# Kernel tuning notes

Hardware: AMD Instinct MI355X
Metric: run time of the kernel (lower is better)

## Reference

```python
import jax, jax.numpy as jnp
import numpy as np

B, C, H, Wd = 4096, 32, 14, 14
ENC_DIM = 512
ATT_DIM = 128


def setup_inputs() -> dict:
    key = jax.random.key(0)
    ks = jax.random.split(key, 10)
    s = 0.05
    return {
        "img_features": jax.random.normal(ks[0], (B, C, H, Wd), jnp.float32),
        "prev_hidden": jax.random.normal(ks[1], (B, ENC_DIM), jnp.float32),
        "W_w": jax.random.normal(ks[2], (ATT_DIM, C), jnp.float32) * s,
        "W_b": jnp.zeros((ATT_DIM,), jnp.float32),
        "U_w": jax.random.normal(ks[3], (ATT_DIM, ENC_DIM), jnp.float32) * s,
        "U_b": jnp.zeros((ATT_DIM,), jnp.float32),
        "v_w": jax.random.normal(ks[4], (1, ATT_DIM), jnp.float32) * s,
        "v_b": jnp.zeros((1,), jnp.float32),
        "fb_w": jax.random.normal(ks[5], (C, ENC_DIM), jnp.float32) * s,
        "fb_b": jnp.zeros((C,), jnp.float32),
    }


def reference(img_features, prev_hidden, W_w, W_b, U_w, U_b, v_w, v_b, fb_w, fb_b):
    b = img_features.shape[0]
    c = img_features.shape[1]
    # [B, C, H, W] -> [B, P, C] where P = H*W (spatial positions)
    img_parts = img_features.reshape(b, c, -1).transpose(0, 2, 1)
    W_s = jnp.einsum('bpc,ac->bpa', img_parts, W_w) + W_b          # [B, P, 128]
    U_h = prev_hidden @ U_w.T + U_b                                 # [B, 128]
    att = jnp.tanh(W_s + U_h[:, None, :])                           # [B, P, 128]
    score = jnp.einsum('bpa,a->bp', att, v_w[0]) + v_b[0]           # [B, P]
    att_weights = jax.nn.softmax(score, axis=1)                     # softmax over spatial
    context = jnp.einsum('bpc,bp->bc', img_parts, att_weights)      # [B, 32]
    beta = jax.nn.sigmoid(prev_hidden @ fb_w.T + fb_b)              # [B, 32]
    context = context * beta
    return (context, att_weights)
```

## Files before the change

kernel.cpp:

```cpp
#include <hip/hip_runtime.h>
#include <hip/hip_bf16.h>


typedef __attribute__((ext_vector_type(8))) short short8;
typedef __attribute__((ext_vector_type(8))) __bf16 bf16x8;
typedef __attribute__((ext_vector_type(4))) float floatx4;
typedef __attribute__((ext_vector_type(4))) unsigned int uint4v;

#define K2E 2.8853900817779268f

#if __has_builtin(__builtin_amdgcn_exp2f)
#define EXP2F(x) __builtin_amdgcn_exp2f(x)
#else
#define EXP2F(x) __expf(0.6931471805599453f * (x))
#endif

static __device__ __forceinline__ float bf2f(unsigned short u) {
    union { unsigned int i; float f; } v; v.i = ((unsigned int)u) << 16; return v.f;
}
static __device__ __forceinline__ unsigned short f2bf(float f) {
    union { float f; unsigned int i; } v; v.f = f;
    unsigned int r = v.i + 0x7FFFu + ((v.i >> 16) & 1u);
    return (unsigned short)(r >> 16);
}
static __device__ __forceinline__ float sigmoid_rcp(float x) {
    return __builtin_amdgcn_rcpf(1.0f + __expf(-x));
}
static __device__ __forceinline__ void split_trunc8(const float* src, bf16x8* hi, bf16x8* lo) {
    uint4v u0 = *(const uint4v*)src;
    uint4v u1 = *(const uint4v*)(src + 4);
    unsigned int fb[8], lb[8];
#pragma unroll
    for (int j = 0; j < 4; j++) { fb[j] = u0[j]; fb[4 + j] = u1[j]; }
#pragma unroll
    for (int k = 0; k < 8; k++) {
        float x = __uint_as_float(fb[k]);
        float h = __uint_as_float(fb[k] & 0xFFFF0000u);
        lb[k] = __float_as_uint(x - h);
    }
    uint4v hp, lp;
#pragma unroll
    for (int j = 0; j < 4; j++) {
        hp[j] = __builtin_amdgcn_perm(fb[2 * j + 1], fb[2 * j], 0x07060302u);
        lp[j] = __builtin_amdgcn_perm(lb[2 * j + 1], lb[2 * j], 0x07060302u);
    }
    *hi = __builtin_bit_cast(bf16x8, hp);
    *lo = __builtin_bit_cast(bf16x8, lp);
}

__global__ __launch_bounds__(256) void k1_gemm(
    const float* __restrict__ hidden,
    const float* __restrict__ U_w, const float* __restrict__ fb_w,
    const float* __restrict__ W_w,
    const float* __restrict__ U_b, const float* __restrict__ W_b,
    const float* __restrict__ fb_b,
    float* __restrict__ uh_out, float* __restrict__ beta_out,
    unsigned short* __restrict__ Whi,
    float* __restrict__ partial, int nsplit, int direct)
{
    __shared__ float s_part[4 * 2560];
    const int tid = threadIdx.x;
    {
        const int gi = blockIdx.x * 256 + tid;
        if (gi < 4096) Whi[gi] = f2bf(W_w[gi] * K2E);
    }
    const int wave = tid >> 6, lane = tid & 63, quad = lane >> 4, l16 = lane & 15;
    const int mtile = blockIdx.x / nsplit;
    const int kblock = 512 / nsplit;
    const int ks0 = (blockIdx.x % nsplit) * kblock + wave * (kblock >> 2);
    const int ksteps = kblock >> 7;
    const int arow = mtile * 16 + l16;

    floatx4 acc[10];
#pragma unroll
    for (int i = 0; i < 10; i++) acc[i] = (floatx4)(0.0f);

    for (int ksi = 0; ksi < ksteps; ksi++) {
        const int e0 = ks0 + ksi * 32 + quad * 8;
        bf16x8 ah, al;
        split_trunc8(hidden + (size_t)arow * 512 + e0, &ah, &al);
#pragma unroll
        for (int n = 0; n < 10; n++) {
            const float* bsrc = (n < 8)
                ? (U_w  + (size_t)(n * 16 + l16) * 512 + e0)
                : (fb_w + (size_t)((n - 8) * 16 + l16) * 512 + e0);
            bf16x8 bh, bl;
            split_trunc8(bsrc, &bh, &bl);
            acc[n] = __builtin_amdgcn_mfma_f32_16x16x32_bf16(ah, bl, acc[n], 0, 0, 0);
            acc[n] = __builtin_amdgcn_mfma_f32_16x16x32_bf16(al, bh, acc[n], 0, 0, 0);
            acc[n] = __builtin_amdgcn_mfma_f32_16x16x32_bf16(ah, bh, acc[n], 0, 0, 0);
        }
    }
#pragma unroll
    for (int n = 0; n < 10; n++)
#pragma unroll
        for (int r = 0; r < 4; r++)
            s_part[wave * 2560 + (quad * 4 + r) * 160 + n * 16 + l16] = acc[n][r];
    __syncthreads();

#pragma unroll
    for (int j = 0; j < 10; j++) {
        const int i = tid + j * 256;
        float v = s_part[i] + s_part[2560 + i] + s_part[5120 + i] + s_part[7680 + i];
        if (direct) {
            const int m = mtile * 16 + i / 160, col = i % 160;
            if (col < 128) uh_out[(size_t)m * 128 + col] = K2E * (v + U_b[col] + W_b[col]);
            else beta_out[(size_t)m * 32 + (col - 128)] = sigmoid_rcp(v + fb_b[col - 128]);
        } else {
            partial[(size_t)blockIdx.x * 2560 + i] = v;
        }
    }
}

__global__ __launch_bounds__(256) void k1b_reduce(
    const float* __restrict__ partial,
    const float* __restrict__ U_b, const float* __restrict__ W_b,
    const float* __restrict__ fb_b,
    float* __restrict__ uh_out, float* __restrict__ beta_out, int nsplit)
{
    const int idx = blockIdx.x * 256 + threadIdx.x;
    const int mt = idx / 640;
    const int r4 = (idx - mt * 640) * 4;
    floatx4 v = (floatx4)(0.0f);
    for (int s = 0; s < nsplit; s++) {
        const floatx4 p = *(const floatx4*)(partial + (size_t)(mt * nsplit + s) * 2560 + r4);
#pragma unroll
        for (int j = 0; j < 4; j++) v[j] += p[j];
    }
    const int m = mt * 16 + r4 / 160, col = r4 % 160;
    if (col < 128) {
        const floatx4 ub = *(const floatx4*)(U_b + col);
        const floatx4 wb = *(const floatx4*)(W_b + col);
        floatx4 o;
#pragma unroll
        for (int j = 0; j < 4; j++) o[j] = K2E * (v[j] + ub[j] + wb[j]);
        *(floatx4*)(uh_out + (size_t)m * 128 + col) = o;
    } else {
        const floatx4 fb = *(const floatx4*)(fb_b + (col - 128));
        floatx4 o;
#pragma unroll
        for (int j = 0; j < 4; j++) o[j] = sigmoid_rcp(v[j] + fb[j]);
        *(floatx4*)(beta_out + (size_t)m * 32 + (col - 128)) = o;
    }
}

#define HSTR 40

__global__ __launch_bounds__(256, 4) void k2_attn(
    const float* __restrict__ img,
    const unsigned short* __restrict__ Whi,
    const float* __restrict__ v_w,
    const float* __restrict__ uh,
    const float* __restrict__ beta,
    float* __restrict__ out)
{
    __shared__ __align__(16) unsigned short s_imgh[208 * HSTR];
    __shared__ float s_score[208];
    __shared__ float s_red[4];
    __shared__ float s_ctx[4][32];

    const int tid = threadIdx.x;
    const int b = blockIdx.x;
    const int wave = tid >> 6, lane = tid & 63, quad = lane >> 4, l16 = lane & 15;

    if (tid < 196) {
        const size_t base = (size_t)b * 6272 + tid;
#pragma unroll
        for (int g = 0; g < 4; g++) {
            unsigned int hb[8];
#pragma unroll
            for (int j = 0; j < 8; j++) {
                unsigned int u = __float_as_uint(img[base + (size_t)(8 * g + j) * 196]);
                hb[j] = u + 0x7FFFu + ((u >> 16) & 1u);
            }
            uint4v hp;
#pragma unroll
            for (int j = 0; j < 4; j++)
                hp[j] = __builtin_amdgcn_perm(hb[2 * j + 1], hb[2 * j], 0x07060302u);
            *(uint4v*)&s_imgh[tid * HSTR + g * 8] = hp;
        }
    } else {
        for (int i = tid - 196; i < 12 * HSTR; i += 60) s_imgh[196 * HSTR + i] = 0;
        if (tid < 208) s_score[tid] = 0.0f;
    }

    float uaR[8], va2R[8], sv = 0.0f;
#pragma unroll
    for (int nt = 0; nt < 8; nt++) {
        uaR[nt] = uh[(size_t)b * 128 + nt * 16 + l16];
        float v = v_w[nt * 16 + l16];
        sv += v;
        va2R[nt] = -2.0f * v;
    }
    sv += __shfl_xor(sv, 1); sv += __shfl_xor(sv, 2);
    sv += __shfl_xor(sv, 4); sv += __shfl_xor(sv, 8);
    __syncthreads();

    float esum = 0.0f;
    for (int mt = wave; mt < 13; mt += 4) {
        bf16x8 a = *(const bf16x8*)&s_imgh[(mt * 16 + l16) * HSTR + quad * 8];
        float sc4[4] = {0.f, 0.f, 0.f, 0.f};
#pragma unroll
        for (int nt = 0; nt < 8; nt++) {
            bf16x8 bh = *(const bf16x8*)(Whi + (nt * 16 + l16) * 32 + quad * 8);
            const float ua = uaR[nt];
            floatx4 d = {ua, ua, ua, ua};
            d = __builtin_amdgcn_mfma_f32_16x16x32_bf16(a, bh, d, 0, 0, 0);
#pragma unroll
            for (int r = 0; r < 4; r++) {
                float e = EXP2F(d[r]);
                float rr = __builtin_amdgcn_rcpf(1.0f + e);
                sc4[r] = __builtin_fmaf(va2R[nt], rr, sc4[r]);
            }
        }
#pragma unroll
        for (int r = 0; r < 4; r++) {
            float s = sc4[r];
            s += __shfl_xor(s, 1); s += __shfl_xor(s, 2);
            s += __shfl_xor(s, 4); s += __shfl_xor(s, 8);
            const int p = mt * 16 + quad * 4 + r;
            if (l16 == 0 && p < 196) {
                float e = __expf(sv + s);
                s_score[p] = e;
                esum += e;
            }
        }
    }
    esum += __shfl_xor(esum, 16);
    esum += __shfl_xor(esum, 32);
    if (lane == 0) s_red[wave] = esum;
    __syncthreads();

    const float tot = s_red[0] + s_red[1] + s_red[2] + s_red[3];
    const float rtot = __builtin_amdgcn_rcpf(tot);
    if (tid < 196)
        out[131072 + (size_t)b * 196 + tid] = s_score[tid] * rtot;

    {
        const int c = lane & 31;
        const int po = wave * 2 + (lane >> 5);
        float acc = 0.0f;
#pragma unroll 5
        for (int j = 0; j < 25; j++) {
            const int p = po + j * 8;
            acc = __builtin_fmaf(bf2f(s_imgh[p * HSTR + c]), s_score[p], acc);
        }
        acc += __shfl_xor(acc, 32);
        if ((lane >> 5) == 0) s_ctx[wave][c] = acc;
    }
    __syncthreads();
    if (tid < 32) {
        const float v = s_ctx[0][tid] + s_ctx[1][tid] + s_ctx[2][tid] + s_ctx[3][tid];
        out[(size_t)b * 32 + tid] = v * rtot * beta[(size_t)b * 32 + tid];
    }
}

extern "C" void kernel_launch(void* const* d_in, const int* in_sizes, int n_in,
                              void* d_out, int out_size, void* d_ws, size_t ws_size,
                              hipStream_t stream) {
    const float* img    = (const float*)d_in[0];
    const float* hidden = (const float*)d_in[1];
    const float* W_w    = (const float*)d_in[2];
    const float* W_b    = (const float*)d_in[3];
    const float* U_w    = (const float*)d_in[4];
    const float* U_b    = (const float*)d_in[5];
    const float* v_w    = (const float*)d_in[6];
    const float* fb_w   = (const float*)d_in[8];
    const float* fb_b   = (const float*)d_in[9];
    float* out = (float*)d_out;

    float* uh_ws   = (float*)d_ws;
    float* beta_ws = uh_ws + 4096 * 128;
    unsigned short* Whi = (unsigned short*)(beta_ws + 4096 * 32);
    float* partial = (float*)(Whi + 4096);
    const size_t fixed_bytes = ((char*)partial) - ((char*)d_ws);

    int nsplit = 1, direct = 1;
    if (ws_size >= fixed_bytes + (size_t)256 * 4 * 2560 * 4) { nsplit = 4; direct = 0; }
    else if (ws_size >= fixed_bytes + (size_t)256 * 2 * 2560 * 4) { nsplit = 2; direct = 0; }
    else if (ws_size >= fixed_bytes + (size_t)256 * 1 * 2560 * 4) { nsplit = 1; direct = 0; }

    k1_gemm<<<dim3(256 * nsplit), dim3(256), 0, stream>>>(
        hidden, U_w, fb_w, W_w, U_b, W_b, fb_b,
        uh_ws, beta_ws, Whi, partial, nsplit, direct);
    if (!direct)
        k1b_reduce<<<dim3(640), dim3(256), 0, stream>>>(
            partial, U_b, W_b, fb_b, uh_ws, beta_ws, nsplit);
    k2_attn<<<dim3(4096), dim3(256), 0, stream>>>(img, Whi, v_w, uh_ws, beta_ws, out);
}
```

Baseline: 202.0 us.

## Double-buffer image staging via async global_load_lds, two batches per block

Result: slower. 218.7 us (+8.3%).

```diff
diff --git a/kernel.cpp b/kernel.cpp
--- a/kernel.cpp
+++ b/kernel.cpp
@@ -14,6 +14,9 @@
 #else
 #define EXP2F(x) __expf(0.6931471805599453f * (x))
 #endif
+
+typedef __attribute__((address_space(3))) unsigned int as3_u32;
+typedef const __attribute__((address_space(1))) unsigned int as1_u32;
 
 static __device__ __forceinline__ float bf2f(unsigned short u) {
     union { unsigned int i; float f; } v; v.i = ((unsigned int)u) << 16; return v.f;
@@ -144,61 +147,42 @@
     }
 }
 
-#define HSTR 40
-
-__global__ __launch_bounds__(256, 4) void k2_attn(
-    const float* __restrict__ img,
+#define SRAW 6284
+
+static __device__ __forceinline__ void stage_img(
+    const float* __restrict__ img, int bb, float* dst, int wave, int lane)
+{
+    const unsigned int* g = (const unsigned int*)(img + (size_t)bb * 6272);
+    for (int ch = wave; ch < 98; ch += 4) {
+        __builtin_amdgcn_global_load_lds(
+            (as1_u32*)(g + ch * 64 + lane),
+            (as3_u32*)((unsigned int*)dst + ch * 64),
+            4, 0, 0);
+    }
+}
+
+static __device__ __forceinline__ void attn_batch(
+    int bb, const float* __restrict__ sraw,
     const unsigned short* __restrict__ Whi,
-    const float* __restrict__ v_w,
-    const float* __restrict__ uh,
-    const float* __restrict__ beta,
-    float* __restrict__ out)
-{
-    __shared__ __align__(16) unsigned short s_imgh[208 * HSTR];
-    __shared__ float s_score[208];
-    __shared__ float s_red[4];
-    __shared__ float s_ctx[4][32];
-
-    const int tid = threadIdx.x;
-    const int b = blockIdx.x;
-    const int wave = tid >> 6, lane = tid & 63, quad = lane >> 4, l16 = lane & 15;
-
-    if (tid < 196) {
-        const size_t base = (size_t)b * 6272 + tid;
-#pragma unroll
-        for (int g = 0; g < 4; g++) {
-            unsigned int hb[8];
-#pragma unroll
-            for (int j = 0; j < 8; j++) {
-                unsigned int u = __float_as_uint(img[base + (size_t)(8 * g + j) * 196]);
-                hb[j] = u + 0x7FFFu + ((u >> 16) & 1u);
-            }
-            uint4v hp;
-#pragma unroll
-            for (int j = 0; j < 4; j++)
-                hp[j] = __builtin_amdgcn_perm(hb[2 * j + 1], hb[2 * j], 0x07060302u);
-            *(uint4v*)&s_imgh[tid * HSTR + g * 8] = hp;
-        }
-    } else {
-        for (int i = tid - 196; i < 12 * HSTR; i += 60) s_imgh[196 * HSTR + i] = 0;
-        if (tid < 208) s_score[tid] = 0.0f;
-    }
-
-    float uaR[8], va2R[8], sv = 0.0f;
-#pragma unroll
-    for (int nt = 0; nt < 8; nt++) {
-        uaR[nt] = uh[(size_t)b * 128 + nt * 16 + l16];
-        float v = v_w[nt * 16 + l16];
-        sv += v;
-        va2R[nt] = -2.0f * v;
-    }
-    sv += __shfl_xor(sv, 1); sv += __shfl_xor(sv, 2);
-    sv += __shfl_xor(sv, 4); sv += __shfl_xor(sv, 8);
-    __syncthreads();
-
+    const float* __restrict__ beta, float* __restrict__ out,
+    float* s_score, float* s_red, float (*s_ctx)[32],
+    const float* uaR, const float* va2R, float sv,
+    int tid, int wave, int lane, int quad, int l16)
+{
     float esum = 0.0f;
     for (int mt = wave; mt < 13; mt += 4) {
-        bf16x8 a = *(const bf16x8*)&s_imgh[(mt * 16 + l16) * HSTR + quad * 8];
+        unsigned int hb[8];
+#pragma unroll
+        for (int j = 0; j < 8; j++) {
+            unsigned int u = __float_as_uint(sraw[(quad * 8 + j) * 196 + mt * 16 + l16]);
+            hb[j] = u + 0x7FFFu + ((u >> 16) & 1u);
+        }
+        uint4v hp;
+#pragma unroll
+        for (int j = 0; j < 4; j++)
+            hp[j] = __builtin_amdgcn_perm(hb[2 * j + 1], hb[2 * j], 0x07060302u);
+        bf16x8 a = __builtin_bit_cast(bf16x8, hp);
+
         float sc4[4] = {0.f, 0.f, 0.f, 0.f};
 #pragma unroll
         for (int nt = 0; nt < 8; nt++) {
@@ -234,7 +218,7 @@
     const float tot = s_red[0] + s_red[1] + s_red[2] + s_red[3];
     const float rtot = __builtin_amdgcn_rcpf(tot);
     if (tid < 196)
-        out[131072 + (size_t)b * 196 + tid] = s_score[tid] * rtot;
+        out[131072 + (size_t)bb * 196 + tid] = s_score[tid] * rtot;
 
     {
         const int c = lane & 31;
@@ -243,7 +227,7 @@
 #pragma unroll 5
         for (int j = 0; j < 25; j++) {
             const int p = po + j * 8;
-            acc = __builtin_fmaf(bf2f(s_imgh[p * HSTR + c]), s_score[p], acc);
+            acc = __builtin_fmaf(sraw[c * 196 + p], s_score[p], acc);
         }
         acc += __shfl_xor(acc, 32);
         if ((lane >> 5) == 0) s_ctx[wave][c] = acc;
@@ -251,8 +235,60 @@
     __syncthreads();
     if (tid < 32) {
         const float v = s_ctx[0][tid] + s_ctx[1][tid] + s_ctx[2][tid] + s_ctx[3][tid];
-        out[(size_t)b * 32 + tid] = v * rtot * beta[(size_t)b * 32 + tid];
-    }
+        out[(size_t)bb * 32 + tid] = v * rtot * beta[(size_t)bb * 32 + tid];
+    }
+}
+
+__global__ __launch_bounds__(256, 3) void k2_attn(
+    const float* __restrict__ img,
+    const unsigned short* __restrict__ Whi,
+    const float* __restrict__ v_w,
+    const float* __restrict__ uh,
+    const float* __restrict__ beta,
+    float* __restrict__ out)
+{
+    __shared__ __align__(16) float s_raw[2][SRAW];
+    __shared__ float s_score[208];
+    __shared__ float s_red[4];
+    __shared__ float s_ctx[4][32];
+
+    const int tid = threadIdx.x;
+    const int b = blockIdx.x;
+    const int wave = tid >> 6, lane = tid & 63, quad = lane >> 4, l16 = lane & 15;
+
+    if (tid < 12) { s_raw[0][6272 + tid] = 0.0f; s_raw[1][6272 + tid] = 0.0f; }
+    if (tid >= 196 && tid < 208) s_score[tid] = 0.0f;
+    stage_img(img, b, s_raw[0], wave, lane);
+
+    float va2R[8], sv = 0.0f;
+#pragma unroll
+    for (int nt = 0; nt < 8; nt++) {
+        float v = v_w[nt * 16 + l16];
+        sv += v;
+        va2R[nt] = -2.0f * v;
+    }
+    sv += __shfl_xor(sv, 1); sv += __shfl_xor(sv, 2);
+    sv += __shfl_xor(sv, 4); sv += __shfl_xor(sv, 8);
+
+    float uaR[8];
+#pragma unroll
+    for (int nt = 0; nt < 8; nt++) uaR[nt] = uh[(size_t)b * 128 + nt * 16 + l16];
+
+    __syncthreads();
+
+    stage_img(img, b + 2048, s_raw[1], wave, lane);
+
+    attn_batch(b, s_raw[0], Whi, beta, out, s_score, s_red, s_ctx,
+               uaR, va2R, sv, tid, wave, lane, quad, l16);
+
+#pragma unroll
+    for (int nt = 0; nt < 8; nt++)
+        uaR[nt] = uh[(size_t)(b + 2048) * 128 + nt * 16 + l16];
+
+    __syncthreads();
+
+    attn_batch(b + 2048, s_raw[1], Whi, beta, out, s_score, s_red, s_ctx,
+               uaR, va2R, sv, tid, wave, lane, quad, l16);
 }
 
 extern "C" void kernel_launch(void* const* d_in, const int* in_sizes, int n_in,
@@ -286,5 +322,5 @@
     if (!direct)
         k1b_reduce<<<dim3(640), dim3(256), 0, stream>>>(
             partial, U_b, W_b, fb_b, uh_ws, beta_ws, nsplit);
-    k2_attn<<<dim3(4096), dim3(256), 0, stream>>>(img, Whi, v_w, uh_ws, beta_ws, out);
-}
+    k2_attn<<<dim3(2048), dim3(256), 0, stream>>>(img, Whi, v_w, uh_ws, beta_ws, out);
+}
```
